# Optimization experiments

Hardware: AMD Instinct MI355X
Metric: run time of the kernel (lower is better)

## Reference

```python
import jax, jax.numpy as jnp
import numpy as np

K = 5      # neighborhood size (k in torch module)
D_DIL = 4  # dilation (d in torch module)


def _neighbor_indices(H, W, k, d):
    # Matches torch: offsets = range(-(k//2)*d, k*(d//2)+1, d); pairs (i,j) added to (x,y), clamped.
    offs = np.arange(-(k // 2) * d, k * (d // 2) + 1, d)
    pairs = np.array([(i, j) for i in offs for j in offs])  # (k2, 2): i -> x offset, j -> y offset
    y, x = np.meshgrid(np.arange(H), np.arange(W), indexing='ij')
    xi = np.clip(x[None, :, :] + pairs[:, 0, None, None], 0, W - 1)  # (k2, H, W)
    yi = np.clip(y[None, :, :] + pairs[:, 1, None, None], 0, H - 1)  # (k2, H, W)
    return jnp.asarray(yi, jnp.int32), jnp.asarray(xi, jnp.int32)


def _safe_l2(diff):
    # L2 norm over last axis with a grad-safe zero (norm at 0 has subgradient 0, like torch).
    ss = jnp.sum(diff * diff, axis=-1)
    safe = jnp.where(ss > 0, ss, 1.0)
    return jnp.where(ss > 0, jnp.sqrt(safe), 0.0)


def setup_inputs() -> dict:
    key = jax.random.key(0)
    des = jax.random.normal(key, (2, 64, 384, 384), dtype=jnp.float32)
    return {"des": des}


def reference(des):
    B, D, H, W = des.shape
    k2 = K * K
    # per-pixel std of descriptor over channel dim
    mu = jnp.mean(des, axis=1)                                  # (B, H, W)
    s_abs = jnp.sqrt(jnp.mean(des * des, axis=1) - mu * mu)     # (B, H, W)

    des_p = jnp.transpose(des, (0, 2, 3, 1))                    # (B, H, W, D)
    yi, xi = _neighbor_indices(H, W, K, D_DIL)                  # (k2, H, W) each

    # Stream over k^2 neighbor offsets, accumulating L2 distances (avoids (B,k2,H,W,D) blowup).
    def body(acc, idx):
        y, x = idx
        nb = des_p[:, y, x, :]                                  # (B, H, W, D) gather
        return acc + _safe_l2(des_p - nb), None

    acc0 = jnp.zeros((B, H, W), des.dtype)
    acc, _ = jax.lax.scan(body, acc0, (yi, xi))
    s_rel = acc / k2                                            # (B, H, W)

    s_raw = s_abs * s_rel
    s = s_raw / (s_raw + 1.0)
    return s[:, None, :, :]                                     # (B, 1, H, W)
```

## Files before the change

### kernel.cpp

```cpp
#include <hip/hip_runtime.h>

#define HH 384
#define WW 384
#define HWP (HH * WW)
#define DD 64
#define BB 2
#define NG2 8

#define TX 32
#define TY 8
#define LR 24
#define LC 48
#define LN (LR * LC)
#define NT 128
#define SPT (LN / NT)
#define NBX (WW / TX)
#define NBY (HH / TY)
#define NWG (NBX * NBY * BB)

typedef __fp16 h2v __attribute__((ext_vector_type(2)));
union h4 { uint2 u; h2v h[2]; };

#if __has_builtin(__builtin_amdgcn_fdot2)
#define DOT4(acc, a, b)                                           \
    acc = __builtin_amdgcn_fdot2((a).h[0], (b).h[0], acc, false);   \
    acc = __builtin_amdgcn_fdot2((a).h[1], (b).h[1], acc, false)
#else
#define DOT4(acc, a, b)                                     \
    acc = fmaf((float)(a).h[0].x, (float)(b).h[0].x, acc);   \
    acc = fmaf((float)(a).h[0].y, (float)(b).h[0].y, acc);   \
    acc = fmaf((float)(a).h[1].x, (float)(b).h[1].x, acc);   \
    acc = fmaf((float)(a).h[1].y, (float)(b).h[1].y, acc)
#endif

__global__ __launch_bounds__(256) void stats_pack_k(const float* __restrict__ des,
                                                    uint4* __restrict__ hp4,
                                                    float* __restrict__ ssq,
                                                    float* __restrict__ smm) {
    int idx = blockIdx.x * 256 + threadIdx.x;
    int b = idx / HWP;
    int p = idx - b * HWP;
    const float* base = des + (size_t)b * DD * HWP + p;
    uint4* hb = hp4 + (size_t)b * NG2 * HWP + p;
    float ss = 0.f, s0 = 0.f;
#pragma unroll 2
    for (int g = 0; g < NG2; ++g) {
        float v0 = base[(size_t)(8 * g + 0) * HWP];
        float v1 = base[(size_t)(8 * g + 1) * HWP];
        float v2 = base[(size_t)(8 * g + 2) * HWP];
        float v3 = base[(size_t)(8 * g + 3) * HWP];
        float v4 = base[(size_t)(8 * g + 4) * HWP];
        float v5 = base[(size_t)(8 * g + 5) * HWP];
        float v6 = base[(size_t)(8 * g + 6) * HWP];
        float v7 = base[(size_t)(8 * g + 7) * HWP];
        ss = fmaf(v0, v0, ss); ss = fmaf(v1, v1, ss);
        ss = fmaf(v2, v2, ss); ss = fmaf(v3, v3, ss);
        ss = fmaf(v4, v4, ss); ss = fmaf(v5, v5, ss);
        ss = fmaf(v6, v6, ss); ss = fmaf(v7, v7, ss);
        s0 += ((v0 + v1) + (v2 + v3)) + ((v4 + v5) + (v6 + v7));
        h4 a, c;
        a.h[0] = __builtin_amdgcn_cvt_pkrtz(v0, v1);
        a.h[1] = __builtin_amdgcn_cvt_pkrtz(v2, v3);
        c.h[0] = __builtin_amdgcn_cvt_pkrtz(v4, v5);
        c.h[1] = __builtin_amdgcn_cvt_pkrtz(v6, v7);
        uint4 w; w.x = a.u.x; w.y = a.u.y; w.z = c.u.x; w.w = c.u.y;
        hb[(size_t)g * HWP] = w;
    }
    ssq[idx] = ss;
    smm[idx] = s0;
}

__global__ __launch_bounds__(NT) void ssd_k(const uint4* __restrict__ hp4,
                                            const float* __restrict__ ssq,
                                            const float* __restrict__ smm,
                                            float* __restrict__ out) {
    __shared__ uint4 lds[2][LN];
    const int tx = threadIdx.x;
    const int ty = threadIdx.y;
    const int tid = ty * 32 + tx;

    int bid = blockIdx.x;
    int swz = (bid & 7) * 144 + (bid >> 3);
    int b  = swz / (NBX * NBY);
    int r0 = swz % (NBX * NBY);
    int by = r0 / NBX;
    int bx = r0 - by * NBX;
    const int x0 = bx * TX, y0 = by * TY;
    const int x = x0 + tx;
    const int y = y0 + ty;

    int goff[SPT];
#pragma unroll
    for (int k = 0; k < SPT; ++k) {
        int i = tid + NT * k;
        int r = i / LC, c = i - (i / LC) * LC;
        int gy = y0 + r - 8; gy = gy < 0 ? 0 : (gy > HH - 1 ? HH - 1 : gy);
        int gx = x0 + c - 8; gx = gx < 0 ? 0 : (gx > WW - 1 ? WW - 1 : gx);
        goff[k] = gy * WW + gx;
    }

    const uint4* hb = hp4 + (size_t)b * NG2 * HWP;

    auto STAGE = [&](int g, int bb) {
        const uint4* p = hb + (size_t)g * HWP;
        uint4 rg[SPT];
#pragma unroll
        for (int k = 0; k < SPT; ++k) rg[k] = p[goff[k]];
#pragma unroll
        for (int k = 0; k < SPT; ++k) lds[bb][tid + NT * k] = rg[k];
    };

    float accA[25], accB[25];
#pragma unroll
    for (int n = 0; n < 25; ++n) { accA[n] = 0.f; accB[n] = 0.f; }

    const int base = ty * LC + tx;
    auto COMPUTE = [&](int bb) {
        const uint4* L = lds[bb];
        uint4 cc0 = L[base + 8 * LC + 8];
        uint4 cc1 = L[base + 12 * LC + 8];
        h4 cA0, cA1, cB0, cB1;
        cA0.u.x = cc0.x; cA0.u.y = cc0.y; cA1.u.x = cc0.z; cA1.u.y = cc0.w;
        cB0.u.x = cc1.x; cB0.u.y = cc1.y; cB1.u.x = cc1.z; cB1.u.y = cc1.w;
#pragma unroll
        for (int m = 0; m < 6; ++m)
#pragma unroll
            for (int j = 0; j < 5; ++j) {
                uint4 v = L[base + (4 * m) * LC + 4 * j];
                h4 va, vb;
                va.u.x = v.x; va.u.y = v.y; vb.u.x = v.z; vb.u.y = v.w;
                if (m < 5) {
                    int n = m * 5 + j;
                    DOT4(accA[n], cA0, va);
                    DOT4(accA[n], cA1, vb);
                }
                if (m >= 1) {
                    int n = (m - 1) * 5 + j;
                    DOT4(accB[n], cB0, va);
                    DOT4(accB[n], cB1, vb);
                }
            }
    };

    STAGE(0, 0);
    __syncthreads();
#pragma unroll 1
    for (int g = 0; g < NG2; g += 2) {
        if (g + 1 < NG2) STAGE(g + 1, 1);
        COMPUTE(0);
        __syncthreads();
        if (g + 2 < NG2) STAGE(g + 2, 0);
        COMPUTE(1);
        __syncthreads();
    }

    float* lsq = (float*)&lds[0][0];
    {
        const float* sp = ssq + (size_t)b * HWP;
        float r[SPT];
#pragma unroll
        for (int k = 0; k < SPT; ++k) r[k] = sp[goff[k]];
#pragma unroll
        for (int k = 0; k < SPT; ++k) lsq[tid + NT * k] = r[k];
    }
    __syncthreads();

    float sv[6][5];
#pragma unroll
    for (int m = 0; m < 6; ++m)
#pragma unroll
        for (int j = 0; j < 5; ++j)
            sv[m][j] = lsq[base + (4 * m) * LC + 4 * j];

    int yc[6], xc[5];
#pragma unroll
    for (int m = 0; m < 6; ++m) {
        int yy = y - 8 + 4 * m; yc[m] = yy < 0 ? 0 : (yy > HH - 1 ? HH - 1 : yy);
    }
#pragma unroll
    for (int j = 0; j < 5; ++j) {
        int xx = x - 8 + 4 * j; xc[j] = xx < 0 ? 0 : (xx > WW - 1 ? WW - 1 : xx);
    }

#pragma unroll
    for (int a = 0; a < 2; ++a) {
        const int py = y + 4 * a;
        const float* acc = a ? accB : accA;
        float ssA = sv[2 + a][2];
        float mu = smm[(size_t)b * HWP + py * WW + x] * (1.0f / 64);
        float var = ssA * (1.0f / 64) - mu * mu;
        float sabs = sqrtf(fmaxf(var, 0.f));
        float L = 0.f;
#pragma unroll
        for (int m = 0; m < 5; ++m)
#pragma unroll
            for (int j = 0; j < 5; ++j) {
                float ssB = sv[m + a][j];
                float d2 = fmaxf(ssA + ssB - 2.f * acc[m * 5 + j], 0.f);
                float sq = sqrtf(d2);
                L += (yc[m + a] == py && xc[j] == x) ? 0.f : sq;
            }
        float srel = L * (1.0f / 25);
        float sraw = sabs * srel;
        out[(size_t)b * HWP + py * WW + x] = sraw / (sraw + 1.f);
    }
}

extern "C" void kernel_launch(void* const* d_in, const int* in_sizes, int n_in,
                              void* d_out, int out_size, void* d_ws, size_t ws_size,
                              hipStream_t stream) {
    const float* des = (const float*)d_in[0];
    float* out = (float*)d_out;

    uint4* hp4 = (uint4*)d_ws;
    float* ssq = (float*)(hp4 + (size_t)BB * NG2 * HWP);
    float* smm = ssq + (size_t)BB * HWP;

    stats_pack_k<<<dim3((BB * HWP) / 256), dim3(256), 0, stream>>>(des, hp4, ssq, smm);
    ssd_k<<<dim3(NWG), dim3(TX, 4), 0, stream>>>(hp4, ssq, smm, out);
}
```

Baseline: 57.89 us.

## Stage neighborhood tiles with direct global-to-LDS loads and vmcnt-based pipelining

Replaces the register round-trip staging of fp16 descriptor tiles with `global_load_lds` 16-byte copies that write straight into shared memory. The double-buffered loop now issues two stages up front and, each iteration, waits on `vmcnt` only for the older stage before a raw barrier. The next stage is issued after compute finishes reading the buffer. The aim is to cut VGPR pressure and the LDS-store instructions, and to keep one stage of global loads in flight during compute. The cost is reliance on hand-written waitcnt counts tied to SPT=9, and on wave-uniform LDS base addressing for the async copies.

```diff
diff --git a/kernel.cpp b/kernel.cpp
--- a/kernel.cpp
+++ b/kernel.cpp
@@ -32,6 +32,14 @@
     acc = fmaf((float)(a).h[1].x, (float)(b).h[1].x, acc);   \
     acc = fmaf((float)(a).h[1].y, (float)(b).h[1].y, acc)
 #endif
+
+__device__ __forceinline__ void gl_lds16(const uint4* g, uint4* l) {
+    __builtin_amdgcn_global_load_lds(
+        (const __attribute__((address_space(1))) unsigned int*)(const void*)g,
+        (__attribute__((address_space(3))) unsigned int*)(void*)l, 16, 0, 0);
+}
+
+#define FENCE() asm volatile("" ::: "memory")
 
 __global__ __launch_bounds__(256) void stats_pack_k(const float* __restrict__ des,
                                                     uint4* __restrict__ hp4,
@@ -103,11 +111,9 @@
 
     auto STAGE = [&](int g, int bb) {
         const uint4* p = hb + (size_t)g * HWP;
-        uint4 rg[SPT];
-#pragma unroll
-        for (int k = 0; k < SPT; ++k) rg[k] = p[goff[k]];
-#pragma unroll
-        for (int k = 0; k < SPT; ++k) lds[bb][tid + NT * k] = rg[k];
+#pragma unroll
+        for (int k = 0; k < SPT; ++k)
+            gl_lds16(p + goff[k], &lds[bb][tid + NT * k]);
     };
 
     float accA[25], accB[25];
@@ -143,15 +149,18 @@
     };
 
     STAGE(0, 0);
-    __syncthreads();
+    STAGE(1, 1);
 #pragma unroll 1
-    for (int g = 0; g < NG2; g += 2) {
-        if (g + 1 < NG2) STAGE(g + 1, 1);
-        COMPUTE(0);
-        __syncthreads();
-        if (g + 2 < NG2) STAGE(g + 2, 0);
-        COMPUTE(1);
-        __syncthreads();
+    for (int g = 0; g < NG2; ++g) {
+        if (g < NG2 - 1) { asm volatile("s_waitcnt vmcnt(9)" ::: "memory"); }
+        else             { asm volatile("s_waitcnt vmcnt(0)" ::: "memory"); }
+        __builtin_amdgcn_s_barrier();
+        FENCE();
+        COMPUTE(g & 1);
+        FENCE();
+        __builtin_amdgcn_s_barrier();
+        FENCE();
+        if (g + 2 < NG2) STAGE(g + 2, g & 1);
     }
 
     float* lsq = (float*)&lds[0][0];
```

New measurement: 47.72 us (median of 2 runs). 17.6% less time.
